# Optimization experiments

Measured on AMD Instinct MI355X. Metric: run time of the kernel, lower is better.

The kernel has to match this reference:

```python
import jax, jax.numpy as jnp
import numpy as np

N_AGENTS = 16      # args['num_agents']
BATCH = 8192       # args['n_rollout_threads'] -> number of independent graphs
OBS = 64           # cent_obs_shape[0] // n_nodes
HID = 128          # args['hidden_sizes'][0]
N_LAYERS = 2       # args['n_layers']
USE_RES = True     # args['use_res']


def _build_edges():
    # complete graph (no self loops) per graph, block-diagonal over BATCH graphs
    i, j = np.meshgrid(np.arange(N_AGENTS), np.arange(N_AGENTS), indexing='ij')
    m = i != j
    bs, bd = i[m], j[m]                      # [240]
    off = (np.arange(BATCH) * N_AGENTS)[:, None]
    src = (bs[None, :] + off).ravel().astype(np.int32)  # [BATCH*240]
    dst = (bd[None, :] + off).ravel().astype(np.int32)
    return src, dst


def setup_inputs() -> dict:
    key = jax.random.key(0)
    ks = jax.random.split(key, 5)
    N = BATCH * N_AGENTS
    src, dst = _build_edges()
    return {
        'cent_obs': jax.random.normal(ks[0], (N, OBS), jnp.float32),
        'w_emb': jax.random.normal(ks[1], (OBS, HID), jnp.float32) / np.sqrt(OBS).astype(np.float32),
        'b_emb': jnp.zeros((HID,), jnp.float32),
        'w_gcn': jax.random.normal(ks[2], (N_LAYERS, HID, HID), jnp.float32) / np.sqrt(HID).astype(np.float32),
        'b_gcn': jnp.zeros((N_LAYERS, HID), jnp.float32),
        'w_fc1': jax.random.normal(ks[3], (HID, 1), jnp.float32) / np.sqrt(HID).astype(np.float32),
        'b_fc1': jnp.zeros((1,), jnp.float32),
        'edge_src': jnp.asarray(src),
        'edge_dst': jnp.asarray(dst),
    }


def reference(cent_obs, w_emb, b_emb, w_gcn, b_gcn, w_fc1, b_fc1, edge_src, edge_dst):
    N = cent_obs.shape[0]
    # embedding_in
    x = cent_obs @ w_emb + b_emb                           # [N, HID]
    # GCNConv normalization with added self-loops (PyG default, sym norm)
    loop = jnp.arange(N, dtype=edge_src.dtype)
    src = jnp.concatenate([edge_src, loop])
    dst = jnp.concatenate([edge_dst, loop])
    deg = jax.ops.segment_sum(jnp.ones_like(dst, dtype=x.dtype), dst, num_segments=N)
    inv_sqrt = jax.lax.rsqrt(deg)
    norm = (inv_sqrt[src] * inv_sqrt[dst])[:, None]        # [E+N, 1]
    for l in range(N_LAYERS):
        h = x @ w_gcn[l]                                   # linear transform
        agg = jax.ops.segment_sum(h[src] * norm, dst, num_segments=N) + b_gcn[l]
        x = jnp.tanh(agg + x if USE_RES else agg)
    value = x @ w_fc1 + b_fc1                              # [N, 1]
    value = value.reshape(BATCH, -1)                       # [BATCH, n_nodes]
    return value.mean(axis=1).reshape(-1, 1)               # [BATCH, 1]
```

## Files before the change

kernel.cpp:

```cpp
#include <hip/hip_runtime.h>


#define N_GRAPHS 8192
#define BLOCK    512
#define GPB      8
#define NBLOCKS  (N_GRAPHS / GPB)

typedef __attribute__((ext_vector_type(8))) short short8;
typedef __attribute__((ext_vector_type(4))) float floatx4;

#define MFMA16(a, b, c) __builtin_amdgcn_mfma_f32_16x16x32_bf16((a), (b), (c), 0, 0, 0)

#define EMB_LO   1024
#define GCN_BASE 2048
#define GCN_LO   2048

union fragu { unsigned int u[4]; short8 s8; };

__device__ __forceinline__ unsigned fbits(float x) {
  union { float f; unsigned u; } v; v.f = x; return v.u;
}
__device__ __forceinline__ float bitsf(unsigned u) {
  union { float f; unsigned u; } v; v.u = u; return v.f;
}
__device__ __forceinline__ void bsplit(float x, short& hi, short& lo) {
  unsigned hb = fbits(x) & 0xFFFF0000u;
  hi = (short)(hb >> 16);
  lo = (short)(fbits(x - bitsf(hb)) >> 16);
}
__device__ __forceinline__ unsigned hpack(unsigned b_odd, unsigned b_even) {
  return __builtin_amdgcn_perm(b_odd, b_even, 0x07060302u);
}
__device__ __forceinline__ void mk_frags(float4 a, float4 b, short8& hi, short8& lo) {
  fragu H, L;
  H.u[0] = hpack(fbits(a.y), fbits(a.x));
  H.u[1] = hpack(fbits(a.w), fbits(a.z));
  H.u[2] = hpack(fbits(b.y), fbits(b.x));
  H.u[3] = hpack(fbits(b.w), fbits(b.z));
  float l0 = a.x - bitsf(fbits(a.x) & 0xFFFF0000u);
  float l1 = a.y - bitsf(fbits(a.y) & 0xFFFF0000u);
  float l2 = a.z - bitsf(fbits(a.z) & 0xFFFF0000u);
  float l3 = a.w - bitsf(fbits(a.w) & 0xFFFF0000u);
  float l4 = b.x - bitsf(fbits(b.x) & 0xFFFF0000u);
  float l5 = b.y - bitsf(fbits(b.y) & 0xFFFF0000u);
  float l6 = b.z - bitsf(fbits(b.z) & 0xFFFF0000u);
  float l7 = b.w - bitsf(fbits(b.w) & 0xFFFF0000u);
  L.u[0] = hpack(fbits(l1), fbits(l0));
  L.u[1] = hpack(fbits(l3), fbits(l2));
  L.u[2] = hpack(fbits(l5), fbits(l4));
  L.u[3] = hpack(fbits(l7), fbits(l6));
  hi = H.s8; lo = L.s8;
}
__device__ __forceinline__ float fast_tanh(float z) {
  float e = __expf(2.0f * z);
  return 1.0f - __fdividef(2.0f, e + 1.0f);
}

__global__ __launch_bounds__(256) void gcn_prep(
    const float* __restrict__ w_emb, const float* __restrict__ w_gcn,
    unsigned short* __restrict__ wsS)
{
  int f = blockIdx.x * 256 + threadIdx.x;
  if (f >= 5120) return;
  const float* src;
  int hi_f, lo_f;
  if (f < 1024) {
    int kc = f >> 9, nt = (f >> 6) & 7, L = f & 63;
    int k0 = kc * 32 + (L >> 4) * 8, n = nt * 16 + (L & 15);
    src = w_emb + k0 * 128 + n;
    hi_f = f; lo_f = f + EMB_LO;
  } else {
    int f2 = f - 1024;
    int l = f2 >> 11, r = f2 & 2047;
    int kc = r >> 9, nt = (r >> 6) & 7, L = r & 63;
    int k0 = kc * 32 + (L >> 4) * 8, n = nt * 16 + (L & 15);
    src = w_gcn + l * 16384 + k0 * 128 + n;
    hi_f = GCN_BASE + l * 4096 + r; lo_f = hi_f + GCN_LO;
  }
  #pragma unroll
  for (int j = 0; j < 8; ++j) {
    short h, l_;
    bsplit(src[j * 128], h, l_);
    wsS[hi_f * 8 + j] = (unsigned short)h;
    wsS[lo_f * 8 + j] = (unsigned short)l_;
  }
}

__global__ __launch_bounds__(BLOCK, 6) void gcn_main(
    const float* __restrict__ obs,
    const float* __restrict__ b_emb,
    const float* __restrict__ b_gcn,
    const float* __restrict__ w_fc1,
    const float* __restrict__ b_fc1,
    const short8* __restrict__ tab,
    float* __restrict__ out)
{
  __shared__ short8 sEmb[2048];
  __shared__ short  sA[2 * 4 * 16 * 40];
  __shared__ float  sH[8][132];

  const int tid = threadIdx.x;
  const int w   = tid >> 6;
  const int L   = tid & 63;
  const int c16 = L & 15;
  const int q   = L >> 4;
  const int kh  = L >> 5;
  const int group = blockIdx.x * GPB + w;

  const float* op = obs + (group * 16 + c16) * 64 + q * 8;
  float4 o00 = *(const float4*)(op);
  float4 o01 = *(const float4*)(op + 4);
  float4 o10 = *(const float4*)(op + 32);
  float4 o11 = *(const float4*)(op + 36);

  #pragma unroll
  for (int i = 0; i < 4; ++i) sEmb[i * BLOCK + tid] = tab[i * BLOCK + tid];
  {
    unsigned int* za = (unsigned int*)sA;
    #pragma unroll
    for (int z = 0; z < 3; ++z) {
      int i = z * BLOCK + tid;
      if (i < 1280) {
        int reg = i / 160, rm = i - reg * 160;
        int r8 = rm / 20, cw = rm - r8 * 20;
        za[reg * 320 + (r8 + 8) * 20 + cw] = 0;
      }
    }
  }

  floatx4 x[8];
  #pragma unroll
  for (int nt = 0; nt < 8; ++nt) {
    float b = b_emb[nt * 16 + c16];
    x[nt] = (floatx4){b, b, b, b};
  }
  __syncthreads();

  #pragma unroll
  for (int kc = 0; kc < 2; ++kc) {
    short8 ah, al;
    mk_frags(kc ? o10 : o00, kc ? o11 : o01, ah, al);
    #pragma unroll
    for (int nt = 0; nt < 8; ++nt) {
      int idx = kc * 512 + nt * 64 + L;
      short8 bh = sEmb[idx];
      short8 bl = sEmb[idx + EMB_LO];
      x[nt] = MFMA16(ah, bh, x[nt]);
      x[nt] = MFMA16(al, bh, x[nt]);
      x[nt] = MFMA16(ah, bl, x[nt]);
    }
  }

  #pragma unroll 1
  for (int l = 0; l < 2; ++l) {
    const short8* tb = tab + GCN_BASE + l * 4096 + w * 64 + L;
    short8 bhc[2], blc[2];
    bhc[0] = tb[0];    blc[0] = tb[GCN_LO];
    bhc[1] = tb[512];  blc[1] = tb[512 + GCN_LO];

    #pragma unroll
    for (int nt = 0; nt < 8; ++nt) {
      float s = x[nt][0] + x[nt][1] + x[nt][2] + x[nt][3];
      s += __shfl_xor(s, 16);
      s += __shfl_xor(s, 32);
      float v = s * 0.0625f;
      unsigned hb = fbits(v) & 0xFFFF0000u;
      unsigned vb = (kh == 0) ? hb : fbits(v - bitsf(hb));
      unsigned nb = (unsigned)__shfl_xor((int)vb, 1);
      if (((c16 & 1) | (q & 1)) == 0) {
        unsigned pw = hpack(nb, vb);
        int kc = nt >> 1, qp = ((nt & 1) << 1) | (c16 >> 3), j = c16 & 7;
        int hw = kh * 2560 + kc * 640 + w * 40 + qp * 8 + j;
        *(unsigned int*)&sA[hw] = pw;
      }
    }
    __syncthreads();

    floatx4 h0 = {0.f, 0.f, 0.f, 0.f};
    floatx4 h1 = {0.f, 0.f, 0.f, 0.f};
    #pragma unroll
    for (int kc = 0; kc < 4; ++kc) {
      short8 bh = bhc[kc & 1], bl = blc[kc & 1];
      if (kc < 2) {
        bhc[kc & 1] = tb[(kc + 2) * 512];
        blc[kc & 1] = tb[(kc + 2) * 512 + GCN_LO];
      }
      short8 ah = *(const short8*)&sA[kc * 640 + c16 * 40 + q * 8];
      short8 al = *(const short8*)&sA[2560 + kc * 640 + c16 * 40 + q * 8];
      floatx4& hh = (kc < 2) ? h0 : h1;
      hh = MFMA16(ah, bh, hh);
      hh = MFMA16(al, bh, hh);
      hh = MFMA16(ah, bl, hh);
    }
    if (q < 2) {
      float bgc = b_gcn[l * 128 + w * 16 + c16];
      #pragma unroll
      for (int r = 0; r < 4; ++r)
        sH[q * 4 + r][w * 16 + c16] = h0[r] + h1[r] + bgc;
    }
    __syncthreads();

    #pragma unroll
    for (int nt = 0; nt < 8; ++nt) {
      float z = sH[w][nt * 16 + c16];
      x[nt][0] = fast_tanh(x[nt][0] + z);
      x[nt][1] = fast_tanh(x[nt][1] + z);
      x[nt][2] = fast_tanh(x[nt][2] + z);
      x[nt][3] = fast_tanh(x[nt][3] + z);
    }
  }

  float v = 0.f;
  #pragma unroll
  for (int nt = 0; nt < 8; ++nt) {
    float wf = w_fc1[nt * 16 + c16];
    v = fmaf(x[nt][0] + x[nt][1] + x[nt][2] + x[nt][3], wf, v);
  }
  #pragma unroll
  for (int d = 32; d >= 1; d >>= 1) v += __shfl_xor(v, d);
  if (L == 0) out[group] = v * 0.0625f + b_fc1[0];
}

extern "C" void kernel_launch(void* const* d_in, const int* in_sizes, int n_in,
                              void* d_out, int out_size, void* d_ws, size_t ws_size,
                              hipStream_t stream) {
  const float* obs    = (const float*)d_in[0];
  const float* w_emb  = (const float*)d_in[1];
  const float* b_emb  = (const float*)d_in[2];
  const float* w_gcn  = (const float*)d_in[3];
  const float* b_gcn  = (const float*)d_in[4];
  const float* w_fc1  = (const float*)d_in[5];
  const float* b_fc1  = (const float*)d_in[6];
  float* out = (float*)d_out;

  gcn_prep<<<20, 256, 0, stream>>>(w_emb, w_gcn, (unsigned short*)d_ws);
  gcn_main<<<NBLOCKS, BLOCK, 0, stream>>>(obs, b_emb, b_gcn, w_fc1, b_fc1,
                                          (const short8*)d_ws, out);
}
```

Baseline: 122.9 us.

## Halve block to 4 graphs, read embedding weights from global, split GCN columns per wave

Shrinks each block from 8 waves/graphs to 4. The embedding weight fragments are now read directly from global/L2 instead of being staged in a 32KB LDS copy, which removes that copy and one barrier. Each wave now computes two 16-column output tiles of the GCN transform over all four k-chunks instead of one tile with a k-split. The change cuts LDS use per block so more blocks can be resident, at the cost of more global weight traffic per wave and a lower launch-bounds occupancy hint.

```diff
diff --git a/kernel.cpp b/kernel.cpp
--- a/kernel.cpp
+++ b/kernel.cpp
@@ -2,8 +2,8 @@
 
 
 #define N_GRAPHS 8192
-#define BLOCK    512
-#define GPB      8
+#define BLOCK    256
+#define GPB      4
 #define NBLOCKS  (N_GRAPHS / GPB)
 
 typedef __attribute__((ext_vector_type(8))) short short8;
@@ -86,7 +86,7 @@
   }
 }
 
-__global__ __launch_bounds__(BLOCK, 6) void gcn_main(
+__global__ __launch_bounds__(BLOCK, 5) void gcn_main(
     const float* __restrict__ obs,
     const float* __restrict__ b_emb,
     const float* __restrict__ b_gcn,
@@ -95,9 +95,8 @@
     const short8* __restrict__ tab,
     float* __restrict__ out)
 {
-  __shared__ short8 sEmb[2048];
-  __shared__ short  sA[2 * 4 * 16 * 40];
-  __shared__ float  sH[8][132];
+  __shared__ short sA[2 * 4 * 16 * 40];
+  __shared__ float sH[4][132];
 
   const int tid = threadIdx.x;
   const int w   = tid >> 6;
@@ -113,17 +112,15 @@
   float4 o10 = *(const float4*)(op + 32);
   float4 o11 = *(const float4*)(op + 36);
 
-  #pragma unroll
-  for (int i = 0; i < 4; ++i) sEmb[i * BLOCK + tid] = tab[i * BLOCK + tid];
   {
     unsigned int* za = (unsigned int*)sA;
     #pragma unroll
-    for (int z = 0; z < 3; ++z) {
+    for (int z = 0; z < 8; ++z) {
       int i = z * BLOCK + tid;
-      if (i < 1280) {
-        int reg = i / 160, rm = i - reg * 160;
-        int r8 = rm / 20, cw = rm - r8 * 20;
-        za[reg * 320 + (r8 + 8) * 20 + cw] = 0;
+      if (i < 1920) {
+        int reg = i / 240, rm = i - reg * 240;
+        int r12 = rm / 20, cw = rm - r12 * 20;
+        za[reg * 320 + (r12 + 4) * 20 + cw] = 0;
       }
     }
   }
@@ -134,7 +131,6 @@
     float b = b_emb[nt * 16 + c16];
     x[nt] = (floatx4){b, b, b, b};
   }
-  __syncthreads();
 
   #pragma unroll
   for (int kc = 0; kc < 2; ++kc) {
@@ -143,8 +139,8 @@
     #pragma unroll
     for (int nt = 0; nt < 8; ++nt) {
       int idx = kc * 512 + nt * 64 + L;
-      short8 bh = sEmb[idx];
-      short8 bl = sEmb[idx + EMB_LO];
+      short8 bh = tab[idx];
+      short8 bl = tab[idx + EMB_LO];
       x[nt] = MFMA16(ah, bh, x[nt]);
       x[nt] = MFMA16(al, bh, x[nt]);
       x[nt] = MFMA16(ah, bl, x[nt]);
@@ -153,10 +149,10 @@
 
   #pragma unroll 1
   for (int l = 0; l < 2; ++l) {
-    const short8* tb = tab + GCN_BASE + l * 4096 + w * 64 + L;
-    short8 bhc[2], blc[2];
-    bhc[0] = tb[0];    blc[0] = tb[GCN_LO];
-    bhc[1] = tb[512];  blc[1] = tb[512 + GCN_LO];
+    const short8* tb0 = tab + GCN_BASE + l * 4096 + (2 * w) * 64 + L;
+    const short8* tb1 = tb0 + 64;
+    short8 bh0 = tb0[0], bl0 = tb0[GCN_LO];
+    short8 bh1 = tb1[0], bl1 = tb1[GCN_LO];
 
     #pragma unroll
     for (int nt = 0; nt < 8; ++nt) {
@@ -180,23 +176,25 @@
     floatx4 h1 = {0.f, 0.f, 0.f, 0.f};
     #pragma unroll
     for (int kc = 0; kc < 4; ++kc) {
-      short8 bh = bhc[kc & 1], bl = blc[kc & 1];
-      if (kc < 2) {
-        bhc[kc & 1] = tb[(kc + 2) * 512];
-        blc[kc & 1] = tb[(kc + 2) * 512 + GCN_LO];
-      }
       short8 ah = *(const short8*)&sA[kc * 640 + c16 * 40 + q * 8];
       short8 al = *(const short8*)&sA[2560 + kc * 640 + c16 * 40 + q * 8];
-      floatx4& hh = (kc < 2) ? h0 : h1;
-      hh = MFMA16(ah, bh, hh);
-      hh = MFMA16(al, bh, hh);
-      hh = MFMA16(ah, bl, hh);
-    }
-    if (q < 2) {
-      float bgc = b_gcn[l * 128 + w * 16 + c16];
+      short8 cbh0 = bh0, cbl0 = bl0, cbh1 = bh1, cbl1 = bl1;
+      if (kc < 3) {
+        bh0 = tb0[(kc + 1) * 512]; bl0 = tb0[(kc + 1) * 512 + GCN_LO];
+        bh1 = tb1[(kc + 1) * 512]; bl1 = tb1[(kc + 1) * 512 + GCN_LO];
+      }
+      h0 = MFMA16(ah, cbh0, h0); h1 = MFMA16(ah, cbh1, h1);
+      h0 = MFMA16(al, cbh0, h0); h1 = MFMA16(al, cbh1, h1);
+      h0 = MFMA16(ah, cbl0, h0); h1 = MFMA16(ah, cbl1, h1);
+    }
+    if (q == 0) {
+      float bg0 = b_gcn[l * 128 + (2 * w) * 16 + c16];
+      float bg1 = b_gcn[l * 128 + (2 * w + 1) * 16 + c16];
       #pragma unroll
-      for (int r = 0; r < 4; ++r)
-        sH[q * 4 + r][w * 16 + c16] = h0[r] + h1[r] + bgc;
+      for (int r = 0; r < 4; ++r) {
+        sH[r][(2 * w) * 16 + c16]     = h0[r] + bg0;
+        sH[r][(2 * w + 1) * 16 + c16] = h1[r] + bg1;
+      }
     }
     __syncthreads();
 
```

Measured after the change: 123.6 us. No clear change (+0.6%).
